# Performance work log

Hardware: AMD Instinct MI355X
Metric: run time of the kernel (lower is better)

Reference implementation:

```python
import jax, jax.numpy as jnp
import numpy as np

D_MODEL = 2048
N_EXPERTS = 8
TOP_K = 2
FFN_HIDDEN = int(D_MODEL * 1.5)  # 3072, matches int(d_model*1.5)


def setup_inputs() -> dict:
    key = jax.random.key(0)
    k_x, k_r, k_g, k_u, k_d = jax.random.split(key, 5)
    B, L = 4, 4096
    s_in = 1.0 / np.sqrt(D_MODEL)
    s_hid = 1.0 / np.sqrt(FFN_HIDDEN)
    return {
        "x": jax.random.normal(k_x, (B, L, D_MODEL), dtype=jnp.float32),
        # nn.Linear weights are stored (out_features, in_features)
        "router_w": jax.random.uniform(k_r, (N_EXPERTS, D_MODEL), jnp.float32, -s_in, s_in),
        "gate_w": jax.random.uniform(k_g, (N_EXPERTS, FFN_HIDDEN, D_MODEL), jnp.float32, -s_in, s_in),
        "up_w": jax.random.uniform(k_u, (N_EXPERTS, FFN_HIDDEN, D_MODEL), jnp.float32, -s_in, s_in),
        "down_w": jax.random.uniform(k_d, (N_EXPERTS, D_MODEL, FFN_HIDDEN), jnp.float32, -s_hid, s_hid),
    }


def reference(x, router_w, gate_w, up_w, down_w):
    B, L, D = x.shape
    x_flat = x.reshape(-1, D)                                   # [N, D]

    router_logits = x_flat @ router_w.T                          # [N, E]
    router_probs = jax.nn.softmax(router_logits, axis=-1)
    top_k_probs, top_k_idx = jax.lax.top_k(router_probs, TOP_K)  # [N, K]
    top_k_probs = top_k_probs / jnp.sum(top_k_probs, axis=-1, keepdims=True)

    # combine[n, e] = sum_k top_k_probs[n,k] * (top_k_idx[n,k] == e)
    onehot = jax.nn.one_hot(top_k_idx, N_EXPERTS, dtype=x.dtype)  # [N, K, E]
    combine = jnp.einsum("nk,nke->ne", top_k_probs, onehot)       # [N, E]

    # Masked gather/scatter in the original == weight-0 tokens here; same math.
    output = jnp.zeros_like(x_flat)
    for e in range(N_EXPERTS):
        gate = jax.nn.silu(x_flat @ gate_w[e].T)                  # [N, H]
        up = x_flat @ up_w[e].T                                   # [N, H]
        expert_out = (gate * up) @ down_w[e].T                    # [N, D]
        output = output + combine[:, e:e + 1] * expert_out

    # dropout is identity in eval/reference mode
    return output.reshape(B, L, D)
```

## Files before the change

### kernel.cpp

```cpp
#include <hip/hip_runtime.h>
#include <hip/hip_bf16.h>
#include <cstdint>

#define N_TOK 16384
#define DMODEL 2048
#define FFH    3072
#define NGU    (2 * FFH)
#define NEXP   8
#define ATOT   32768

typedef __bf16 bf16;
typedef __attribute__((ext_vector_type(8))) __bf16 bf16x8;
typedef __attribute__((ext_vector_type(4))) __bf16 bf16x4;
typedef __attribute__((ext_vector_type(4))) float  f32x4;

__device__ __forceinline__ void gl_lds16(const bf16* g, void* l) {
  __builtin_amdgcn_global_load_lds(
      (const __attribute__((address_space(1))) void*)g,
      (__attribute__((address_space(3))) void*)l, 16, 0, 0);
}

__global__ void cvt_f32_bf16(const float* __restrict__ src, bf16* __restrict__ dst, long n4) {
  long i = (long)blockIdx.x * blockDim.x + threadIdx.x;
  if (i >= n4) return;
  const float4 v = ((const float4*)src)[i];
  bf16x4 o;
  o.x = (bf16)v.x; o.y = (bf16)v.y; o.z = (bf16)v.z; o.w = (bf16)v.w;
  ((bf16x4*)dst)[i] = o;
}

__global__ void cvt_guw(const float* __restrict__ gw, const float* __restrict__ uw,
                        bf16* __restrict__ guw) {
  const long i = (long)blockIdx.x * 256 + threadIdx.x;
  const int c8 = (int)(i & 255);
  const long rg = i >> 8;
  const int e = (int)(rg / NGU);
  const int ri = (int)(rg - (long)e * NGU);
  const int hb = ri >> 6, sub = ri & 63;
  const float* src = (sub < 32 ? gw : uw) + ((size_t)e * FFH + hb * 32 + (sub & 31)) * DMODEL + c8 * 8;
  const float4 v0 = ((const float4*)src)[0];
  const float4 v1 = ((const float4*)src)[1];
  bf16x8 o;
  o[0] = (bf16)v0.x; o[1] = (bf16)v0.y; o[2] = (bf16)v0.z; o[3] = (bf16)v0.w;
  o[4] = (bf16)v1.x; o[5] = (bf16)v1.y; o[6] = (bf16)v1.z; o[7] = (bf16)v1.w;
  *(bf16x8*)(guw + rg * DMODEL + c8 * 8) = o;
}

__global__ void router_k(const float* __restrict__ x, const float* __restrict__ rw,
                         int* __restrict__ tk_e, float* __restrict__ tk_w,
                         int* __restrict__ cnt) {
  const int wv = threadIdx.x >> 6, lane = threadIdx.x & 63;
  const int t = blockIdx.x * 4 + wv;
  const float* xr = x + (size_t)t * DMODEL;
  float acc[NEXP];
#pragma unroll
  for (int e = 0; e < NEXP; ++e) acc[e] = 0.f;
  for (int k = lane; k < DMODEL; k += 64) {
    const float xv = xr[k];
#pragma unroll
    for (int e = 0; e < NEXP; ++e) acc[e] = fmaf(xv, rw[e * DMODEL + k], acc[e]);
  }
#pragma unroll
  for (int e = 0; e < NEXP; ++e) {
#pragma unroll
    for (int o = 32; o; o >>= 1) acc[e] += __shfl_xor(acc[e], o, 64);
  }
  if (lane == 0) {
    int e0 = 0; float v0 = acc[0];
#pragma unroll
    for (int e = 1; e < NEXP; ++e) if (acc[e] > v0) { v0 = acc[e]; e0 = e; }
    int e1 = -1; float v1 = -1e30f;
#pragma unroll
    for (int e = 0; e < NEXP; ++e) if (e != e0 && acc[e] > v1) { v1 = acc[e]; e1 = e; }
    const float w0 = 1.f / (1.f + __expf(v1 - v0));
    tk_e[t * 2] = e0; tk_e[t * 2 + 1] = e1;
    tk_w[t * 2] = w0; tk_w[t * 2 + 1] = 1.f - w0;
    atomicAdd(&cnt[e0], 1); atomicAdd(&cnt[e1], 1);
  }
}

__global__ void offs_k(const int* __restrict__ cnt, int* __restrict__ offs) {
  if (threadIdx.x == 0) {
    int o = 0;
    for (int e = 0; e < NEXP; ++e) { offs[e] = o; o += cnt[e]; }
  }
}

__global__ void scatter_k(const int* __restrict__ tk_e, const float* __restrict__ tk_w,
                          const int* __restrict__ offs, int* __restrict__ cnt2,
                          int* __restrict__ tok_list, float* __restrict__ w_list,
                          int* __restrict__ aidx) {
  const int t = blockIdx.x * 256 + threadIdx.x;
  if (t >= N_TOK) return;
#pragma unroll
  for (int k = 0; k < 2; ++k) {
    const int e = tk_e[t * 2 + k];
    const int p = atomicAdd(&cnt2[e], 1);
    const int a = offs[e] + p;
    tok_list[a] = t;
    w_list[a] = tk_w[t * 2 + k];
    aidx[t * 2 + k] = a;
  }
}

template<int EPI>
__global__ __launch_bounds__(512, 4) void gemm_moe(
    const bf16* __restrict__ A, const bf16* __restrict__ B,
    bf16* __restrict__ hbuf, float* __restrict__ ybuf,
    const int* __restrict__ tok_list, const int* __restrict__ cnt,
    const int* __restrict__ offs) {
  constexpr int KD = EPI ? FFH : DMODEL;
  constexpr int NT = KD / 32;
  constexpr int BROWS = EPI ? DMODEL : NGU;

  const int e = blockIdx.z;
  const int cn = cnt[e];
  const int mbase = blockIdx.y * 128;
  if (mbase >= cn) return;
  const int offE = offs[e];
  const int nbase = blockIdx.x * 256;

  __shared__ char lds[73728];
  char* const ldsA = lds;
  char* const ldsB = lds + 24576;

  const int tid = threadIdx.x;
  const int wv = tid >> 6, lane = tid & 63;
  const int wr = wv >> 2, wc = wv & 3;

  const int sr = tid >> 2;
  const int swz8 = ((tid & 3) ^ ((tid >> 3) & 3)) * 8;
  const bf16* pA; const bf16* pB[2];
  if (EPI == 0) {
    const int t0 = tok_list[offE + min(mbase + sr, cn - 1)];
    pA = A + (size_t)t0 * KD + swz8;
  } else {
    const int a0 = offE + min(mbase + sr, cn - 1);
    pA = A + (size_t)a0 * KD + swz8;
  }
  pB[0] = B + ((size_t)e * BROWS + nbase + sr) * KD + swz8;
  pB[1] = B + ((size_t)e * BROWS + nbase + 128 + sr) * KD + swz8;

  const int stageDst = wv * 1024;

  const int rswz = ((lane >> 4) ^ ((lane >> 1) & 3)) * 16;
  const int arow = (wr * 64 + (lane & 15)) * 64 + rswz;
  const int brow = (wc * 64 + (lane & 15)) * 64 + rswz;

  const f32x4 zero = {0.f, 0.f, 0.f, 0.f};
  f32x4 acc[4][4];
#pragma unroll
  for (int i = 0; i < 4; ++i)
#pragma unroll
    for (int j = 0; j < 4; ++j) acc[i][j] = zero;

  auto stageA = [&](int buf, int kt) {
    gl_lds16(pA + kt * 32, ldsA + buf * 8192 + stageDst);
  };
  auto stageB = [&](int buf, int half, int kt) {
    gl_lds16(pB[half] + kt * 32, ldsB + buf * 16384 + half * 8192 + stageDst);
  };

  stageA(0, 0); stageB(0, 0, 0); stageB(0, 1, 0);
  stageA(1, 1); stageB(1, 0, 1); stageB(1, 1, 1);
  asm volatile("s_waitcnt vmcnt(3)" ::: "memory");
  __builtin_amdgcn_s_barrier();
  asm volatile("" ::: "memory");

  int cb = 0;
  for (int kt = 0; kt < NT; ++kt) {
    const int sb = (cb + 2 >= 3) ? cb - 1 : cb + 2;
    const char* cA = ldsA + cb * 8192;
    const char* cB = ldsB + cb * 16384;

    bf16x8 a[4], b[4];
#pragma unroll
    for (int i = 0; i < 4; ++i) {
      a[i] = *(const bf16x8*)(cA + i * 1024 + arow);
      b[i] = *(const bf16x8*)(cB + i * 1024 + brow);
    }

    if (kt + 2 < NT) { stageA(sb, kt + 2); stageB(sb, 0, kt + 2); }

    __builtin_amdgcn_s_setprio(1);
#pragma unroll
    for (int nf = 0; nf < 2; ++nf)
#pragma unroll
      for (int mi = 0; mi < 4; ++mi)
        acc[mi][nf] = __builtin_amdgcn_mfma_f32_16x16x32_bf16(a[mi], b[nf], acc[mi][nf], 0, 0, 0);
    __builtin_amdgcn_s_setprio(0);

    if (kt + 2 < NT) { stageB(sb, 1, kt + 2); }

    __builtin_amdgcn_s_setprio(1);
#pragma unroll
    for (int nf = 2; nf < 4; ++nf)
#pragma unroll
      for (int mi = 0; mi < 4; ++mi)
        acc[mi][nf] = __builtin_amdgcn_mfma_f32_16x16x32_bf16(a[mi], b[nf], acc[mi][nf], 0, 0, 0);
    __builtin_amdgcn_s_setprio(0);

    if (kt + 2 < NT) { asm volatile("s_waitcnt vmcnt(3)" ::: "memory"); }
    else             { asm volatile("s_waitcnt vmcnt(0)" ::: "memory"); }
    asm volatile("" ::: "memory");
    __builtin_amdgcn_s_barrier();
    asm volatile("" ::: "memory");

    cb = (cb + 1 == 3) ? 0 : cb + 1;
  }

  const int col = lane & 15;
  const int rb = mbase + wr * 64 + (lane >> 4) * 4;
  if (EPI == 0) {
    const int hb32 = ((nbase + wc * 64) >> 6) * 32;
#pragma unroll
    for (int mi = 0; mi < 4; ++mi)
#pragma unroll
      for (int j = 0; j < 4; ++j) {
        const int row = rb + mi * 16 + j;
        if (row < cn) {
          bf16* hr = hbuf + (size_t)(offE + row) * FFH + hb32 + col;
#pragma unroll
          for (int k = 0; k < 2; ++k) {
            const float g = acc[mi][k][j], u = acc[mi][k + 2][j];
            hr[k * 16] = (bf16)(g / (1.f + __expf(-g)) * u);
          }
        }
      }
  } else {
#pragma unroll
    for (int mi = 0; mi < 4; ++mi)
#pragma unroll
      for (int j = 0; j < 4; ++j) {
        const int row = rb + mi * 16 + j;
        if (row < cn) {
          float* yr = ybuf + (size_t)(offE + row) * DMODEL + nbase + wc * 64 + col;
#pragma unroll
          for (int nf = 0; nf < 4; ++nf) yr[nf * 16] = acc[mi][nf][j];
        }
      }
  }
}

__global__ void combine_k(const float* __restrict__ ybuf, const int* __restrict__ aidx,
                          const float* __restrict__ tk_w, float* __restrict__ out) {
  const int i = blockIdx.x * 256 + threadIdx.x;
  const int t = i >> 9, c = i & 511;
  const int a0 = aidx[t * 2], a1 = aidx[t * 2 + 1];
  const float w0 = tk_w[t * 2], w1 = tk_w[t * 2 + 1];
  const float4 v0 = ((const float4*)(ybuf + (size_t)a0 * DMODEL))[c];
  const float4 v1 = ((const float4*)(ybuf + (size_t)a1 * DMODEL))[c];
  float4 o;
  o.x = w0 * v0.x + w1 * v1.x;
  o.y = w0 * v0.y + w1 * v1.y;
  o.z = w0 * v0.z + w1 * v1.z;
  o.w = w0 * v0.w + w1 * v1.w;
  ((float4*)(out + (size_t)t * DMODEL))[c] = o;
}

extern "C" void kernel_launch(void* const* d_in, const int* in_sizes, int n_in,
                              void* d_out, int out_size, void* d_ws, size_t ws_size,
                              hipStream_t stream) {
  const float* x  = (const float*)d_in[0];
  const float* rw = (const float*)d_in[1];
  const float* gw = (const float*)d_in[2];
  const float* uw = (const float*)d_in[3];
  const float* dw = (const float*)d_in[4];
  float* out = (float*)d_out;

  char* ws = (char*)d_ws;
  size_t o = 0;
  auto alloc = [&](size_t bytes) {
    void* p = ws + o;
    o = (o + bytes + 255) & ~(size_t)255;
    return p;
  };

  const size_t guw_bytes  = (size_t)NEXP * NGU * DMODEL * 2;
  const size_t ybuf_bytes = (size_t)(ATOT + 256) * DMODEL * 4;
  bf16*  xb       = (bf16*)alloc((size_t)N_TOK * DMODEL * 2);
  void*  uni      = alloc(ybuf_bytes > guw_bytes ? ybuf_bytes : guw_bytes);
  bf16*  guw      = (bf16*)uni;
  float* ybuf     = (float*)uni;
  bf16*  dwb      = (bf16*)alloc((size_t)NEXP * DMODEL * FFH * 2);
  bf16*  hbuf     = (bf16*)alloc((size_t)(ATOT + 256) * FFH * 2);
  int*   tok_list = (int*)alloc((ATOT + 256) * 4);
  float* w_list   = (float*)alloc((ATOT + 256) * 4);
  int*   tk_e     = (int*)alloc((size_t)N_TOK * 2 * 4);
  float* tk_w     = (float*)alloc((size_t)N_TOK * 2 * 4);
  int*   aidx     = (int*)alloc((size_t)N_TOK * 2 * 4);
  int*   cnt      = (int*)alloc(64);
  int*   offs     = (int*)alloc(64);
  int*   cnt2     = (int*)alloc(64);

  hipMemsetAsync(cnt, 0, 64, stream);
  hipMemsetAsync(cnt2, 0, 64, stream);

  {
    long n4 = (long)N_TOK * DMODEL / 4;
    cvt_f32_bf16<<<(unsigned)(n4 / 256), 256, 0, stream>>>(x, xb, n4);
  }
  cvt_guw<<<(unsigned)((long)NEXP * NGU * DMODEL / 8 / 256), 256, 0, stream>>>(gw, uw, guw);
  {
    long n4 = (long)NEXP * DMODEL * FFH / 4;
    cvt_f32_bf16<<<(unsigned)(n4 / 256), 256, 0, stream>>>(dw, dwb, n4);
  }

  router_k<<<N_TOK / 4, 256, 0, stream>>>(x, rw, tk_e, tk_w, cnt);
  offs_k<<<1, 64, 0, stream>>>(cnt, offs);
  scatter_k<<<N_TOK / 256, 256, 0, stream>>>(tk_e, tk_w, offs, cnt2, tok_list, w_list, aidx);

  gemm_moe<0><<<dim3(NGU / 256, 128, NEXP), 512, 0, stream>>>(
      xb, guw, hbuf, nullptr, tok_list, cnt, offs);
  gemm_moe<1><<<dim3(DMODEL / 256, 128, NEXP), 512, 0, stream>>>(
      hbuf, dwb, nullptr, ybuf, tok_list, cnt, offs);

  combine_k<<<N_TOK * 512 / 256, 256, 0, stream>>>(ybuf, aidx, tk_w, out);
}
```

Baseline: 2.075 ms.

## Fuse gate/up weight conversion into GEMM and x conversion into router

New measurement: 2.234 ms. +7.7%, slower.

```diff
diff --git a/kernel.cpp b/kernel.cpp
--- a/kernel.cpp
+++ b/kernel.cpp
@@ -5,7 +5,6 @@
 #define N_TOK 16384
 #define DMODEL 2048
 #define FFH    3072
-#define NGU    (2 * FFH)
 #define NEXP   8
 #define ATOT   32768
 
@@ -29,36 +28,29 @@
   ((bf16x4*)dst)[i] = o;
 }
 
-__global__ void cvt_guw(const float* __restrict__ gw, const float* __restrict__ uw,
-                        bf16* __restrict__ guw) {
-  const long i = (long)blockIdx.x * 256 + threadIdx.x;
-  const int c8 = (int)(i & 255);
-  const long rg = i >> 8;
-  const int e = (int)(rg / NGU);
-  const int ri = (int)(rg - (long)e * NGU);
-  const int hb = ri >> 6, sub = ri & 63;
-  const float* src = (sub < 32 ? gw : uw) + ((size_t)e * FFH + hb * 32 + (sub & 31)) * DMODEL + c8 * 8;
-  const float4 v0 = ((const float4*)src)[0];
-  const float4 v1 = ((const float4*)src)[1];
-  bf16x8 o;
-  o[0] = (bf16)v0.x; o[1] = (bf16)v0.y; o[2] = (bf16)v0.z; o[3] = (bf16)v0.w;
-  o[4] = (bf16)v1.x; o[5] = (bf16)v1.y; o[6] = (bf16)v1.z; o[7] = (bf16)v1.w;
-  *(bf16x8*)(guw + rg * DMODEL + c8 * 8) = o;
-}
-
 __global__ void router_k(const float* __restrict__ x, const float* __restrict__ rw,
+                         bf16* __restrict__ xb,
                          int* __restrict__ tk_e, float* __restrict__ tk_w,
                          int* __restrict__ cnt) {
   const int wv = threadIdx.x >> 6, lane = threadIdx.x & 63;
   const int t = blockIdx.x * 4 + wv;
-  const float* xr = x + (size_t)t * DMODEL;
+  const float4* xr = (const float4*)(x + (size_t)t * DMODEL);
+  bf16x4* xbr = (bf16x4*)(xb + (size_t)t * DMODEL);
   float acc[NEXP];
 #pragma unroll
   for (int e = 0; e < NEXP; ++e) acc[e] = 0.f;
-  for (int k = lane; k < DMODEL; k += 64) {
-    const float xv = xr[k];
-#pragma unroll
-    for (int e = 0; e < NEXP; ++e) acc[e] = fmaf(xv, rw[e * DMODEL + k], acc[e]);
+#pragma unroll
+  for (int it = 0; it < DMODEL / 4 / 64; ++it) {
+    const int idx = lane + it * 64;
+    const float4 v = xr[idx];
+    bf16x4 o;
+    o.x = (bf16)v.x; o.y = (bf16)v.y; o.z = (bf16)v.z; o.w = (bf16)v.w;
+    xbr[idx] = o;
+#pragma unroll
+    for (int e = 0; e < NEXP; ++e) {
+      const float4 w = ((const float4*)(rw + e * DMODEL))[idx];
+      acc[e] = fmaf(v.x, w.x, fmaf(v.y, w.y, fmaf(v.z, w.z, fmaf(v.w, w.w, acc[e]))));
+    }
   }
 #pragma unroll
   for (int e = 0; e < NEXP; ++e) {
@@ -103,22 +95,22 @@
   }
 }
 
-template<int EPI>
-__global__ __launch_bounds__(512, 4) void gemm_moe(
-    const bf16* __restrict__ A, const bf16* __restrict__ B,
-    bf16* __restrict__ hbuf, float* __restrict__ ybuf,
-    const int* __restrict__ tok_list, const int* __restrict__ cnt,
-    const int* __restrict__ offs) {
-  constexpr int KD = EPI ? FFH : DMODEL;
-  constexpr int NT = KD / 32;
-  constexpr int BROWS = EPI ? DMODEL : NGU;
-
+__global__ __launch_bounds__(512, 2) void gemm_gu(
+    const bf16* __restrict__ xb, const float* __restrict__ gw, const float* __restrict__ uw,
+    bf16* __restrict__ hbuf, const int* __restrict__ tok_list,
+    const int* __restrict__ cnt, const int* __restrict__ offs) {
+  constexpr int NT = DMODEL / 32;
   const int e = blockIdx.z;
   const int cn = cnt[e];
-  const int mbase = blockIdx.y * 128;
+  const int gy = gridDim.y;
+  const int flat = blockIdx.x + gridDim.x * blockIdx.y;
+  const int q = (gridDim.x * gy) >> 3;
+  const int flat2 = (flat & 7) * q + (flat >> 3);
+  const int nbt = flat2 / gy;
+  const int mbase = (flat2 - nbt * gy) * 128;
   if (mbase >= cn) return;
   const int offE = offs[e];
-  const int nbase = blockIdx.x * 256;
+  const int nbase = nbt * 256;
 
   __shared__ char lds[73728];
   char* const ldsA = lds;
@@ -129,18 +121,159 @@
   const int wr = wv >> 2, wc = wv & 3;
 
   const int sr = tid >> 2;
+  const int c4 = tid & 3;
+  const int swz8 = (c4 ^ ((tid >> 3) & 3)) * 8;
+  const int t0 = tok_list[offE + min(mbase + sr, cn - 1)];
+  const bf16* pA = xb + (size_t)t0 * DMODEL + swz8;
+  const int stageDst = wv * 1024;
+
+  const int R0 = nbase + sr, R1 = nbase + sr + 128;
+  const float* pB0 = ((R0 & 63) < 32 ? gw : uw) +
+      ((size_t)e * FFH + (R0 >> 6) * 32 + (R0 & 31)) * DMODEL + c4 * 8;
+  const float* pB1 = ((R1 & 63) < 32 ? gw : uw) +
+      ((size_t)e * FFH + (R1 >> 6) * 32 + (R1 & 31)) * DMODEL + c4 * 8;
+  const int wchunk = (c4 ^ ((sr >> 1) & 3)) * 16;
+  const int woff0 = sr * 64 + wchunk;
+  const int woff1 = (sr + 128) * 64 + wchunk;
+
+  const int rswz = ((lane >> 4) ^ ((lane >> 1) & 3)) * 16;
+  const int arow = (wr * 64 + (lane & 15)) * 64 + rswz;
+  const int brow = (wc * 64 + (lane & 15)) * 64 + rswz;
+
+  const f32x4 zero = {0.f, 0.f, 0.f, 0.f};
+  f32x4 acc[4][4];
+#pragma unroll
+  for (int i = 0; i < 4; ++i)
+#pragma unroll
+    for (int j = 0; j < 4; ++j) acc[i][j] = zero;
+
+  auto writeB = [&](int buf, const float4& a0, const float4& a1,
+                    const float4& b0, const float4& b1) {
+    bf16x8 w0, w1;
+    w0[0] = (bf16)a0.x; w0[1] = (bf16)a0.y; w0[2] = (bf16)a0.z; w0[3] = (bf16)a0.w;
+    w0[4] = (bf16)a1.x; w0[5] = (bf16)a1.y; w0[6] = (bf16)a1.z; w0[7] = (bf16)a1.w;
+    w1[0] = (bf16)b0.x; w1[1] = (bf16)b0.y; w1[2] = (bf16)b0.z; w1[3] = (bf16)b0.w;
+    w1[4] = (bf16)b1.x; w1[5] = (bf16)b1.y; w1[6] = (bf16)b1.z; w1[7] = (bf16)b1.w;
+    *(bf16x8*)(ldsB + buf * 16384 + woff0) = w0;
+    *(bf16x8*)(ldsB + buf * 16384 + woff1) = w1;
+  };
+
+  {
+    const float4 n0 = ((const float4*)pB0)[0];
+    const float4 n1 = ((const float4*)pB0)[1];
+    const float4 n2 = ((const float4*)pB1)[0];
+    const float4 n3 = ((const float4*)pB1)[1];
+    gl_lds16(pA, ldsA + stageDst);
+    gl_lds16(pA + 32, ldsA + 8192 + stageDst);
+    writeB(0, n0, n1, n2, n3);
+    asm volatile("s_waitcnt vmcnt(1)" ::: "memory");
+    asm volatile("s_waitcnt lgkmcnt(0)" ::: "memory");
+  }
+  __builtin_amdgcn_s_barrier();
+  asm volatile("" ::: "memory");
+
+  int cb = 0;
+  for (int kt = 0; kt < NT; ++kt) {
+    const int nb1 = (cb + 1 == 3) ? 0 : cb + 1;
+    const int nb2 = (nb1 + 1 == 3) ? 0 : nb1 + 1;
+    const char* cA = ldsA + cb * 8192;
+    const char* cB = ldsB + cb * 16384;
+
+    float4 n0, n1, n2, n3;
+    const bool pf1 = (kt + 1 < NT);
+    if (pf1) {
+      const float* s0 = pB0 + (kt + 1) * 32;
+      const float* s1 = pB1 + (kt + 1) * 32;
+      n0 = ((const float4*)s0)[0]; n1 = ((const float4*)s0)[1];
+      n2 = ((const float4*)s1)[0]; n3 = ((const float4*)s1)[1];
+    }
+    if (kt + 2 < NT) gl_lds16(pA + (kt + 2) * 32, ldsA + nb2 * 8192 + stageDst);
+
+    bf16x8 a[4], b01[2], b23[2];
+#pragma unroll
+    for (int i = 0; i < 4; ++i) a[i] = *(const bf16x8*)(cA + i * 1024 + arow);
+#pragma unroll
+    for (int i = 0; i < 2; ++i) b01[i] = *(const bf16x8*)(cB + i * 1024 + brow);
+
+    __builtin_amdgcn_s_setprio(1);
+#pragma unroll
+    for (int nf = 0; nf < 2; ++nf)
+#pragma unroll
+      for (int mi = 0; mi < 4; ++mi)
+        acc[mi][nf] = __builtin_amdgcn_mfma_f32_16x16x32_bf16(a[mi], b01[nf], acc[mi][nf], 0, 0, 0);
+    __builtin_amdgcn_s_setprio(0);
+
+    if (pf1) writeB(nb1, n0, n1, n2, n3);
+
+#pragma unroll
+    for (int i = 0; i < 2; ++i) b23[i] = *(const bf16x8*)(cB + (2 + i) * 1024 + brow);
+    __builtin_amdgcn_s_setprio(1);
+#pragma unroll
+    for (int nf = 0; nf < 2; ++nf)
+#pragma unroll
+      for (int mi = 0; mi < 4; ++mi)
+        acc[mi][nf + 2] = __builtin_amdgcn_mfma_f32_16x16x32_bf16(a[mi], b23[nf], acc[mi][nf + 2], 0, 0, 0);
+    __builtin_amdgcn_s_setprio(0);
+
+    if (kt + 2 < NT) { asm volatile("s_waitcnt vmcnt(1)" ::: "memory"); }
+    else             { asm volatile("s_waitcnt vmcnt(0)" ::: "memory"); }
+    asm volatile("s_waitcnt lgkmcnt(0)" ::: "memory");
+    __builtin_amdgcn_s_barrier();
+    asm volatile("" ::: "memory");
+
+    cb = nb1;
+  }
+
+  const int col = lane & 15;
+  const int rb = mbase + wr * 64 + (lane >> 4) * 4;
+  const int hb32 = ((nbase + wc * 64) >> 6) * 32;
+#pragma unroll
+  for (int mi = 0; mi < 4; ++mi)
+#pragma unroll
+    for (int j = 0; j < 4; ++j) {
+      const int row = rb + mi * 16 + j;
+      if (row < cn) {
+        bf16* hr = hbuf + (size_t)(offE + row) * FFH + hb32 + col;
+#pragma unroll
+        for (int k = 0; k < 2; ++k) {
+          const float g = acc[mi][k][j], u = acc[mi][k + 2][j];
+          hr[k * 16] = (bf16)(g / (1.f + __expf(-g)) * u);
+        }
+      }
+    }
+}
+
+__global__ __launch_bounds__(512, 2) void gemm_dn(
+    const bf16* __restrict__ A, const bf16* __restrict__ B,
+    float* __restrict__ ybuf,
+    const int* __restrict__ cnt, const int* __restrict__ offs) {
+  constexpr int NT = FFH / 32;
+  const int e = blockIdx.z;
+  const int cn = cnt[e];
+  const int gy = gridDim.y;
+  const int flat = blockIdx.x + gridDim.x * blockIdx.y;
+  const int q = (gridDim.x * gy) >> 3;
+  const int flat2 = (flat & 7) * q + (flat >> 3);
+  const int nbt = flat2 / gy;
+  const int mbase = (flat2 - nbt * gy) * 128;
+  if (mbase >= cn) return;
+  const int offE = offs[e];
+  const int nbase = nbt * 256;
+
+  __shared__ char lds[73728];
+  char* const ldsA = lds;
+  char* const ldsB = lds + 24576;
+
+  const int tid = threadIdx.x;
+  const int wv = tid >> 6, lane = tid & 63;
+  const int wr = wv >> 2, wc = wv & 3;
+
+  const int sr = tid >> 2;
   const int swz8 = ((tid & 3) ^ ((tid >> 3) & 3)) * 8;
-  const bf16* pA; const bf16* pB[2];
-  if (EPI == 0) {
-    const int t0 = tok_list[offE + min(mbase + sr, cn - 1)];
-    pA = A + (size_t)t0 * KD + swz8;
-  } else {
-    const int a0 = offE + min(mbase + sr, cn - 1);
-    pA = A + (size_t)a0 * KD + swz8;
-  }
-  pB[0] = B + ((size_t)e * BROWS + nbase + sr) * KD + swz8;
-  pB[1] = B + ((size_t)e * BROWS + nbase + 128 + sr) * KD + swz8;
-
+  const int a0i = offE + min(mbase + sr, cn - 1);
+  const bf16* pA = A + (size_t)a0i * FFH + swz8;
+  const bf16* pB0 = B + ((size_t)e * DMODEL + nbase + sr) * FFH + swz8;
+  const bf16* pB1 = B + ((size_t)e * DMODEL + nbase + 128 + sr) * FFH + swz8;
   const int stageDst = wv * 1024;
 
   const int rswz = ((lane >> 4) ^ ((lane >> 1) & 3)) * 16;
@@ -158,7 +291,7 @@
     gl_lds16(pA + kt * 32, ldsA + buf * 8192 + stageDst);
   };
   auto stageB = [&](int buf, int half, int kt) {
-    gl_lds16(pB[half] + kt * 32, ldsB + buf * 16384 + half * 8192 + stageDst);
+    gl_lds16((half ? pB1 : pB0) + kt * 32, ldsB + buf * 16384 + half * 8192 + stageDst);
   };
 
   stageA(0, 0); stageB(0, 0, 0); stageB(0, 1, 0);
@@ -211,35 +344,17 @@
 
   const int col = lane & 15;
   const int rb = mbase + wr * 64 + (lane >> 4) * 4;
-  if (EPI == 0) {
-    const int hb32 = ((nbase + wc * 64) >> 6) * 32;
-#pragma unroll
-    for (int mi = 0; mi < 4; ++mi)
-#pragma unroll
-      for (int j = 0; j < 4; ++j) {
-        const int row = rb + mi * 16 + j;
-        if (row < cn) {
-          bf16* hr = hbuf + (size_t)(offE + row) * FFH + hb32 + col;
-#pragma unroll
-          for (int k = 0; k < 2; ++k) {
-            const float g = acc[mi][k][j], u = acc[mi][k + 2][j];
-            hr[k * 16] = (bf16)(g / (1.f + __expf(-g)) * u);
-          }
-        }
+#pragma unroll
+  for (int mi = 0; mi < 4; ++mi)
+#pragma unroll
+    for (int j = 0; j < 4; ++j) {
+      const int row = rb + mi * 16 + j;
+      if (row < cn) {
+        float* yr = ybuf + (size_t)(offE + row) * DMODEL + nbase + wc * 64 + col;
+#pragma unroll
+        for (int nf = 0; nf < 4; ++nf) yr[nf * 16] = acc[mi][nf][j];
       }
-  } else {
-#pragma unroll
-    for (int mi = 0; mi < 4; ++mi)
-#pragma unroll
-      for (int j = 0; j < 4; ++j) {
-        const int row = rb + mi * 16 + j;
-        if (row < cn) {
-          float* yr = ybuf + (size_t)(offE + row) * DMODEL + nbase + wc * 64 + col;
-#pragma unroll
-          for (int nf = 0; nf < 4; ++nf) yr[nf * 16] = acc[mi][nf][j];
-        }
-      }
-  }
+    }
 }
 
 __global__ void combine_k(const float* __restrict__ ybuf, const int* __restrict__ aidx,
@@ -276,12 +391,8 @@
     return p;
   };
 
-  const size_t guw_bytes  = (size_t)NEXP * NGU * DMODEL * 2;
-  const size_t ybuf_bytes = (size_t)(ATOT + 256) * DMODEL * 4;
   bf16*  xb       = (bf16*)alloc((size_t)N_TOK * DMODEL * 2);
-  void*  uni      = alloc(ybuf_bytes > guw_bytes ? ybuf_bytes : guw_bytes);
-  bf16*  guw      = (bf16*)uni;
-  float* ybuf     = (float*)uni;
+  float* ybuf     = (float*)alloc((size_t)(ATOT + 256) * DMODEL * 4);
   bf16*  dwb      = (bf16*)alloc((size_t)NEXP * DMODEL * FFH * 2);
   bf16*  hbuf     = (bf16*)alloc((size_t)(ATOT + 256) * FFH * 2);
   int*   tok_list = (int*)alloc((ATOT + 256) * 4);
@@ -296,24 +407,19 @@
   hipMemsetAsync(cnt, 0, 64, stream);
   hipMemsetAsync(cnt2, 0, 64, stream);
 
-  {
-    long n4 = (long)N_TOK * DMODEL / 4;
-    cvt_f32_bf16<<<(unsigned)(n4 / 256), 256, 0, stream>>>(x, xb, n4);
-  }
-  cvt_guw<<<(unsigned)((long)NEXP * NGU * DMODEL / 8 / 256), 256, 0, stream>>>(gw, uw, guw);
+  router_k<<<N_TOK / 4, 256, 0, stream>>>(x, rw, xb, tk_e, tk_w, cnt);
+  offs_k<<<1, 64, 0, stream>>>(cnt, offs);
+  scatter_k<<<N_TOK / 256, 256, 0, stream>>>(tk_e, tk_w, offs, cnt2, tok_list, w_list, aidx);
+
   {
     long n4 = (long)NEXP * DMODEL * FFH / 4;
     cvt_f32_bf16<<<(unsigned)(n4 / 256), 256, 0, stream>>>(dw, dwb, n4);
   }
 
-  router_k<<<N_TOK / 4, 256, 0, stream>>>(x, rw, tk_e, tk_w, cnt);
-  offs_k<<<1, 64, 0, stream>>>(cnt, offs);
-  scatter_k<<<N_TOK / 256, 256, 0, stream>>>(tk_e, tk_w, offs, cnt2, tok_list, w_list, aidx);
-
-  gemm_moe<0><<<dim3(NGU / 256, 128, NEXP), 512, 0, stream>>>(
-      xb, guw, hbuf, nullptr, tok_list, cnt, offs);
-  gemm_moe<1><<<dim3(DMODEL / 256, 128, NEXP), 512, 0, stream>>>(
-      hbuf, dwb, nullptr, ybuf, tok_list, cnt, offs);
+  gemm_gu<<<dim3(FFH * 2 / 256, 128, NEXP), 512, 0, stream>>>(
+      xb, gw, uw, hbuf, tok_list, cnt, offs);
+  gemm_dn<<<dim3(DMODEL / 256, 128, NEXP), 512, 0, stream>>>(
+      hbuf, dwb, ybuf, cnt, offs);
 
   combine_k<<<N_TOK * 512 / 256, 256, 0, stream>>>(ybuf, aidx, tk_w, out);
 }
```
